# Optimization experiments

Measured on AMD Instinct MI355X. Metric: run time of the kernel, lower is better.

## Reference

```python
import jax, jax.numpy as jnp
import numpy as np

B, T, H, HS, E = 4096, 32, 16, 32, 512  # T == block_size == head_size (required by the module's concat-on-time quirk)


def setup_inputs() -> dict:
    key = jax.random.key(0)
    ks = jax.random.split(key, 6)
    s_e = 1.0 / np.sqrt(E).astype(np.float32)
    s_p = 1.0 / np.sqrt(H * HS).astype(np.float32)
    return {
        "x": jax.random.normal(ks[0], (B, T, E), jnp.float32),
        "Wq": jax.random.normal(ks[1], (H, HS, E), jnp.float32) * s_e,  # per-head Linear(E->HS, no bias)
        "Wk": jax.random.normal(ks[2], (H, HS, E), jnp.float32) * s_e,
        "Wv": jax.random.normal(ks[3], (H, HS, E), jnp.float32) * s_e,
        "Wp": jax.random.normal(ks[4], (E, H * HS), jnp.float32) * s_p,  # proj: Linear(H*HS -> E)
        "bp": jnp.zeros((E,), jnp.float32),
    }


def reference(x, Wq, Wk, Wv, Wp, bp):
    # Per-head projections, batched over heads (original loops in Python).
    q = jnp.einsum('bte,hde->bhtd', x, Wq)  # [B,H,T,HS]
    k = jnp.einsum('bte,hde->bhtd', x, Wk)
    v = jnp.einsum('bte,hde->bhtd', x, Wv)
    wei = jnp.einsum('bhtd,bhsd->bhts', q, k) * (HS ** -0.5)  # [B,H,T,T]
    mask = jnp.tril(jnp.ones((T, T), bool))  # causal (T == block_size)
    wei = jnp.where(mask, wei, -jnp.inf)
    wei = jax.nn.softmax(wei, axis=-1)
    # dropout is identity in eval mode
    out = jnp.einsum('bhts,bhsd->bhtd', wei, v)  # [B,H,T,HS]
    # torch.cat(..., dim=1): stack head outputs along the TIME axis -> [B, H*T, HS]
    out = out.reshape(B, H * T, HS)
    out = jnp.swapaxes(out, 1, 2)  # [B, HS, H*T]; valid only because T == HS -> last dim == H*HS == E
    return out @ Wp.T + bp  # [B, HS, E]
```

## Files before the change

### kernel.cpp

```cpp
#include <hip/hip_runtime.h>
#include <stdint.h>

typedef __attribute__((ext_vector_type(8))) short bf16x8;
typedef __attribute__((ext_vector_type(4))) float f32x4;

#define MFMA16(a, b, c) __builtin_amdgcn_mfma_f32_16x16x32_bf16((a), (b), (c), 0, 0, 0)

__device__ __forceinline__ unsigned short f2bf(float f) {
  unsigned int b = __float_as_uint(f);
  b += 0x7FFFu + ((b >> 16) & 1u);
  return (unsigned short)(b >> 16);
}
__device__ __forceinline__ bf16x8 cvt8(const float4 a, const float4 b) {
  bf16x8 r;
  r[0] = (short)f2bf(a.x); r[1] = (short)f2bf(a.y);
  r[2] = (short)f2bf(a.z); r[3] = (short)f2bf(a.w);
  r[4] = (short)f2bf(b.x); r[5] = (short)f2bf(b.y);
  r[6] = (short)f2bf(b.z); r[7] = (short)f2bf(b.w);
  return r;
}
template <bool BF16W>
__device__ __forceinline__ bf16x8 ldw(const void* p, size_t off) {
  if constexpr (BF16W) {
    return *(const bf16x8*)((const unsigned short*)p + off);
  } else {
    const float* f = (const float*)p + off;
    return cvt8(*(const float4*)f, *(const float4*)(f + 4));
  }
}
__device__ __forceinline__ int sw(int row, int chunk) {
  return row * 512 + ((chunk ^ (row & 7)) << 3);
}

__global__ void cvt_weights_k(const float* __restrict__ wq,
                              const float* __restrict__ wk,
                              const float* __restrict__ wv,
                              const float* __restrict__ wp,
                              unsigned short* __restrict__ dst) {
  const int seg = blockIdx.x >> 7;
  const int blk = blockIdx.x & 127;
  const float* src = (seg == 0) ? wq : (seg == 1) ? wk : (seg == 2) ? wv : wp;
  unsigned short* d = dst + (size_t)seg * 262144;
  const int i = (blk * 256 + threadIdx.x) * 8;
  float4 lo = *(const float4*)&src[i];
  float4 hi = *(const float4*)&src[i + 4];
  *(bf16x8*)&d[i] = cvt8(lo, hi);
}

template <bool BF16W>
__global__ __launch_bounds__(256, 2) void qkv_attn_k(
    const float* __restrict__ x,
    const void* __restrict__ wq,
    const void* __restrict__ wk,
    const void* __restrict__ wv,
    float* __restrict__ y) {
  __shared__ __align__(16) unsigned short Xs[32 * 512];
  __shared__ __align__(16) unsigned short Scr[4][3][32 * 40];
  const int tid  = threadIdx.x;
  const int lane = tid & 63;
  const int wave = tid >> 6;
  const int m    = lane & 15;
  const int quad = lane >> 4;
  const int b    = blockIdx.x;

  {
    const float* xg = x + (size_t)b * (32 * 512);
#pragma unroll
    for (int i = 0; i < 8; i++) {
      int c = tid + 256 * i;
      int row = c >> 6, ch = c & 63;
      float4 lo = *(const float4*)&xg[row * 512 + ch * 8];
      float4 hi = *(const float4*)&xg[row * 512 + ch * 8 + 4];
      *(bf16x8*)&Xs[sw(row, ch)] = cvt8(lo, hi);
    }
  }
  __syncthreads();

  unsigned short* Qs = &Scr[wave][0][0];
  unsigned short* Ks = &Scr[wave][1][0];
  unsigned short* Vt = &Scr[wave][2][0];

  for (int hg = 0; hg < 4; hg++) {
    const int h = hg * 4 + wave;
    f32x4 aq[2][2] = {}; f32x4 ak[2][2] = {}; f32x4 av[2][2] = {};
    const size_t wbase = (size_t)(h * 32 + m) * 512 + quad * 8;
#pragma unroll 4
    for (int kk = 0; kk < 16; kk++) {
      const int k0 = kk * 32;
      bf16x8 a0 = *(const bf16x8*)&Xs[sw(m, kk * 4 + quad)];
      bf16x8 a1 = *(const bf16x8*)&Xs[sw(16 + m, kk * 4 + quad)];
      bf16x8 bq0 = ldw<BF16W>(wq, wbase + k0);
      bf16x8 bq1 = ldw<BF16W>(wq, wbase + 16 * 512 + k0);
      bf16x8 bk0 = ldw<BF16W>(wk, wbase + k0);
      bf16x8 bk1 = ldw<BF16W>(wk, wbase + 16 * 512 + k0);
      bf16x8 bv0 = ldw<BF16W>(wv, wbase + k0);
      bf16x8 bv1 = ldw<BF16W>(wv, wbase + 16 * 512 + k0);
      aq[0][0] = MFMA16(a0, bq0, aq[0][0]);
      aq[1][0] = MFMA16(a1, bq0, aq[1][0]);
      aq[0][1] = MFMA16(a0, bq1, aq[0][1]);
      aq[1][1] = MFMA16(a1, bq1, aq[1][1]);
      ak[0][0] = MFMA16(a0, bk0, ak[0][0]);
      ak[1][0] = MFMA16(a1, bk0, ak[1][0]);
      ak[0][1] = MFMA16(a0, bk1, ak[0][1]);
      ak[1][1] = MFMA16(a1, bk1, ak[1][1]);
      av[0][0] = MFMA16(a0, bv0, av[0][0]);
      av[1][0] = MFMA16(a1, bv0, av[1][0]);
      av[0][1] = MFMA16(a0, bv1, av[0][1]);
      av[1][1] = MFMA16(a1, bv1, av[1][1]);
    }
#pragma unroll
    for (int mi = 0; mi < 2; mi++)
#pragma unroll
      for (int ni = 0; ni < 2; ni++)
#pragma unroll
        for (int r = 0; r < 4; r++) {
          int row = mi * 16 + quad * 4 + r;
          int col = ni * 16 + m;
          Qs[row * 40 + col] = f2bf(aq[mi][ni][r]);
          Ks[row * 40 + col] = f2bf(ak[mi][ni][r]);
          Vt[col * 40 + row] = f2bf(av[mi][ni][r]);
        }
    f32x4 sAcc[2][2];
#pragma unroll
    for (int mi = 0; mi < 2; mi++)
#pragma unroll
      for (int ni = 0; ni < 2; ni++) {
        bf16x8 qa = *(const bf16x8*)&Qs[(mi * 16 + m) * 40 + quad * 8];
        bf16x8 kb = *(const bf16x8*)&Ks[(ni * 16 + m) * 40 + quad * 8];
        f32x4 z = {};
        sAcc[mi][ni] = MFMA16(qa, kb, z);
      }
    float invs[2][4];
#pragma unroll
    for (int mi = 0; mi < 2; mi++)
#pragma unroll
      for (int r = 0; r < 4; r++) {
        int t = mi * 16 + quad * 4 + r;
        float s0 = sAcc[mi][0][r] * 0.17677669529663687f;
        float s1 = sAcc[mi][1][r] * 0.17677669529663687f;
        s0 = (m <= t) ? s0 : -1e30f;
        s1 = (16 + m <= t) ? s1 : -1e30f;
        float mx = fmaxf(s0, s1);
#pragma unroll
        for (int off = 1; off < 16; off <<= 1) mx = fmaxf(mx, __shfl_xor(mx, off));
        float e0 = __expf(s0 - mx);
        float e1 = __expf(s1 - mx);
        float sm = e0 + e1;
#pragma unroll
        for (int off = 1; off < 16; off <<= 1) sm += __shfl_xor(sm, off);
        invs[mi][r] = 1.0f / sm;
        Qs[t * 40 + m] = f2bf(e0);
        Qs[t * 40 + 16 + m] = f2bf(e1);
      }
    f32x4 oAcc[2][2];
#pragma unroll
    for (int mi = 0; mi < 2; mi++)
#pragma unroll
      for (int ni = 0; ni < 2; ni++) {
        bf16x8 pa = *(const bf16x8*)&Qs[(mi * 16 + m) * 40 + quad * 8];
        bf16x8 vb = *(const bf16x8*)&Vt[(ni * 16 + m) * 40 + quad * 8];
        f32x4 z = {};
        oAcc[mi][ni] = MFMA16(pa, vb, z);
      }
#pragma unroll
    for (int mi = 0; mi < 2; mi++)
#pragma unroll
      for (int ni = 0; ni < 2; ni++) {
        float4 o;
        o.x = oAcc[mi][ni][0] * invs[mi][0];
        o.y = oAcc[mi][ni][1] * invs[mi][1];
        o.z = oAcc[mi][ni][2] * invs[mi][2];
        o.w = oAcc[mi][ni][3] * invs[mi][3];
        int d = ni * 16 + m;
        int t0 = mi * 16 + quad * 4;
        *(float4*)&y[(size_t)b * 16384 + (size_t)d * 512 + h * 32 + t0] = o;
      }
  }
}

template <bool BF16W>
__global__ __launch_bounds__(256, 2) void proj_k(
    float* __restrict__ y,
    const void* __restrict__ wp,
    const float* __restrict__ bp) {
  __shared__ __align__(16) unsigned short Ys[64 * 512];
  const int tid  = threadIdx.x;
  const int lane = tid & 63;
  const int wave = tid >> 6;
  const int m    = lane & 15;
  const int quad = lane >> 4;
  const size_t rbase = (size_t)blockIdx.x * 64;

  {
    const float* yg = y + rbase * 512;
#pragma unroll
    for (int i = 0; i < 16; i++) {
      int c = tid + 256 * i;
      int row = c >> 6, ch = c & 63;
      float4 lo = *(const float4*)&yg[row * 512 + ch * 8];
      float4 hi = *(const float4*)&yg[row * 512 + ch * 8 + 4];
      *(bf16x8*)&Ys[sw(row, ch)] = cvt8(lo, hi);
    }
  }
  __syncthreads();

  const int nb = wave * 128;
  f32x4 acc[4][8] = {};
#pragma unroll 2
  for (int kk = 0; kk < 16; kk++) {
    bf16x8 a[4];
#pragma unroll
    for (int mi = 0; mi < 4; mi++)
      a[mi] = *(const bf16x8*)&Ys[sw(mi * 16 + m, kk * 4 + quad)];
    const int k0 = kk * 32 + quad * 8;
#pragma unroll
    for (int ni = 0; ni < 8; ni++) {
      bf16x8 bb = ldw<BF16W>(wp, (size_t)(nb + ni * 16 + m) * 512 + k0);
#pragma unroll
      for (int mi = 0; mi < 4; mi++) acc[mi][ni] = MFMA16(a[mi], bb, acc[mi][ni]);
    }
  }
#pragma unroll
  for (int ni = 0; ni < 8; ni++) {
    const int col = nb + ni * 16 + m;
    const float bias = bp[col];
#pragma unroll
    for (int mi = 0; mi < 4; mi++)
#pragma unroll
      for (int r = 0; r < 4; r++) {
        size_t row = rbase + mi * 16 + quad * 4 + r;
        y[row * 512 + col] = acc[mi][ni][r] + bias;
      }
  }
}

extern "C" void kernel_launch(void* const* d_in, const int* in_sizes, int n_in,
                              void* d_out, int out_size, void* d_ws, size_t ws_size,
                              hipStream_t stream) {
  (void)in_sizes; (void)n_in; (void)out_size;
  const float* x  = (const float*)d_in[0];
  const float* wq = (const float*)d_in[1];
  const float* wk = (const float*)d_in[2];
  const float* wv = (const float*)d_in[3];
  const float* wp = (const float*)d_in[4];
  const float* bp = (const float*)d_in[5];
  float* y = (float*)d_out;

  const size_t WE = 262144;
  if (ws_size >= 4 * WE * sizeof(unsigned short)) {
    unsigned short* wb = (unsigned short*)d_ws;
    cvt_weights_k<<<512, 256, 0, stream>>>(wq, wk, wv, wp, wb);
    qkv_attn_k<true><<<4096, 256, 0, stream>>>(x, wb, wb + WE, wb + 2 * WE, y);
    proj_k<true><<<2048, 256, 0, stream>>>(y, wb + 3 * WE, bp);
  } else {
    qkv_attn_k<false><<<4096, 256, 0, stream>>>(x, wq, wk, wv, y);
    proj_k<false><<<2048, 256, 0, stream>>>(y, wp, bp);
  }
}
```

Baseline: 1.284 ms.

## Double-buffer GEMM operand loads and stagger K/head order across blocks

Both the QKV-attention kernel and the projection kernel now software-pipeline their K loops with two register buffers, loading the next K-slice of LDS activations and global weights while MFMAs run on the current one. In addition, each block starts its K loop (and the head-group loop in the attention kernel) at an offset derived from the block index. The offset spreads concurrent blocks across different weight addresses to reduce cache or channel hot-spotting. The cost is higher register pressure, especially in the projection kernel, which now holds two sets of 4+8 operand vectors next to a 128-float accumulator and may spill or lose occupancy.

```diff
diff --git a/kernel.cpp b/kernel.cpp
--- a/kernel.cpp
+++ b/kernel.cpp
@@ -62,6 +62,8 @@
   const int m    = lane & 15;
   const int quad = lane >> 4;
   const int b    = blockIdx.x;
+  const int koff = (blockIdx.x >> 3) & 15;
+  const int hgo  = (blockIdx.x >> 7) & 3;
 
   {
     const float* xg = x + (size_t)b * (32 * 512);
@@ -81,33 +83,52 @@
   unsigned short* Vt = &Scr[wave][2][0];
 
   for (int hg = 0; hg < 4; hg++) {
-    const int h = hg * 4 + wave;
+    const int h = ((hg + hgo) & 3) * 4 + wave;
     f32x4 aq[2][2] = {}; f32x4 ak[2][2] = {}; f32x4 av[2][2] = {};
     const size_t wbase = (size_t)(h * 32 + m) * 512 + quad * 8;
-#pragma unroll 4
-    for (int kk = 0; kk < 16; kk++) {
-      const int k0 = kk * 32;
-      bf16x8 a0 = *(const bf16x8*)&Xs[sw(m, kk * 4 + quad)];
-      bf16x8 a1 = *(const bf16x8*)&Xs[sw(16 + m, kk * 4 + quad)];
-      bf16x8 bq0 = ldw<BF16W>(wq, wbase + k0);
-      bf16x8 bq1 = ldw<BF16W>(wq, wbase + 16 * 512 + k0);
-      bf16x8 bk0 = ldw<BF16W>(wk, wbase + k0);
-      bf16x8 bk1 = ldw<BF16W>(wk, wbase + 16 * 512 + k0);
-      bf16x8 bv0 = ldw<BF16W>(wv, wbase + k0);
-      bf16x8 bv1 = ldw<BF16W>(wv, wbase + 16 * 512 + k0);
-      aq[0][0] = MFMA16(a0, bq0, aq[0][0]);
-      aq[1][0] = MFMA16(a1, bq0, aq[1][0]);
-      aq[0][1] = MFMA16(a0, bq1, aq[0][1]);
-      aq[1][1] = MFMA16(a1, bq1, aq[1][1]);
-      ak[0][0] = MFMA16(a0, bk0, ak[0][0]);
-      ak[1][0] = MFMA16(a1, bk0, ak[1][0]);
-      ak[0][1] = MFMA16(a0, bk1, ak[0][1]);
-      ak[1][1] = MFMA16(a1, bk1, ak[1][1]);
-      av[0][0] = MFMA16(a0, bv0, av[0][0]);
-      av[1][0] = MFMA16(a1, bv0, av[1][0]);
-      av[0][1] = MFMA16(a0, bv1, av[0][1]);
-      av[1][1] = MFMA16(a1, bv1, av[1][1]);
+
+    bf16x8 a0A, a1A, bq0A, bq1A, bk0A, bk1A, bv0A, bv1A;
+    bf16x8 a0B, a1B, bq0B, bq1B, bk0B, bk1B, bv0B, bv1B;
+
+#define LDF(S, idx) { \
+    const int kx = ((idx) + koff) & 15; \
+    const int kb = kx * 32; \
+    a0##S  = *(const bf16x8*)&Xs[sw(m, kx * 4 + quad)]; \
+    a1##S  = *(const bf16x8*)&Xs[sw(16 + m, kx * 4 + quad)]; \
+    bq0##S = ldw<BF16W>(wq, wbase + kb); \
+    bq1##S = ldw<BF16W>(wq, wbase + 16 * 512 + kb); \
+    bk0##S = ldw<BF16W>(wk, wbase + kb); \
+    bk1##S = ldw<BF16W>(wk, wbase + 16 * 512 + kb); \
+    bv0##S = ldw<BF16W>(wv, wbase + kb); \
+    bv1##S = ldw<BF16W>(wv, wbase + 16 * 512 + kb); }
+
+#define MMF(S) { \
+    aq[0][0] = MFMA16(a0##S, bq0##S, aq[0][0]); \
+    aq[1][0] = MFMA16(a1##S, bq0##S, aq[1][0]); \
+    aq[0][1] = MFMA16(a0##S, bq1##S, aq[0][1]); \
+    aq[1][1] = MFMA16(a1##S, bq1##S, aq[1][1]); \
+    ak[0][0] = MFMA16(a0##S, bk0##S, ak[0][0]); \
+    ak[1][0] = MFMA16(a1##S, bk0##S, ak[1][0]); \
+    ak[0][1] = MFMA16(a0##S, bk1##S, ak[0][1]); \
+    ak[1][1] = MFMA16(a1##S, bk1##S, ak[1][1]); \
+    av[0][0] = MFMA16(a0##S, bv0##S, av[0][0]); \
+    av[1][0] = MFMA16(a1##S, bv0##S, av[1][0]); \
+    av[0][1] = MFMA16(a0##S, bv1##S, av[0][1]); \
+    av[1][1] = MFMA16(a1##S, bv1##S, av[1][1]); }
+
+    LDF(A, 0)
+    for (int i = 0; i < 14; i += 2) {
+      LDF(B, i + 1)
+      MMF(A)
+      LDF(A, i + 2)
+      MMF(B)
     }
+    LDF(B, 15)
+    MMF(A)
+    MMF(B)
+#undef LDF
+#undef MMF
+
 #pragma unroll
     for (int mi = 0; mi < 2; mi++)
 #pragma unroll
@@ -190,6 +211,7 @@
   const int m    = lane & 15;
   const int quad = lane >> 4;
   const size_t rbase = (size_t)blockIdx.x * 64;
+  const int koff = (blockIdx.x >> 3) & 15;
 
   {
     const float* yg = y + rbase * 512;
@@ -206,20 +228,40 @@
 
   const int nb = wave * 128;
   f32x4 acc[4][8] = {};
-#pragma unroll 2
-  for (int kk = 0; kk < 16; kk++) {
-    bf16x8 a[4];
-#pragma unroll
-    for (int mi = 0; mi < 4; mi++)
-      a[mi] = *(const bf16x8*)&Ys[sw(mi * 16 + m, kk * 4 + quad)];
-    const int k0 = kk * 32 + quad * 8;
-#pragma unroll
-    for (int ni = 0; ni < 8; ni++) {
-      bf16x8 bb = ldw<BF16W>(wp, (size_t)(nb + ni * 16 + m) * 512 + k0);
-#pragma unroll
-      for (int mi = 0; mi < 4; mi++) acc[mi][ni] = MFMA16(a[mi], bb, acc[mi][ni]);
-    }
-  }
+  bf16x8 aA[4], aB[4], wA[8], wB[8];
+
+#define K2A(S, idx) { \
+    const int kx = ((idx) + koff) & 15; \
+    _Pragma("unroll") \
+    for (int mi = 0; mi < 4; mi++) \
+      a##S[mi] = *(const bf16x8*)&Ys[sw(mi * 16 + m, kx * 4 + quad)]; }
+#define K2W(S, idx) { \
+    const int kx = ((idx) + koff) & 15; \
+    const int kb = kx * 32 + quad * 8; \
+    _Pragma("unroll") \
+    for (int ni = 0; ni < 8; ni++) \
+      w##S[ni] = ldw<BF16W>(wp, (size_t)(nb + ni * 16 + m) * 512 + kb); }
+#define K2MM(S) { \
+    _Pragma("unroll") \
+    for (int ni = 0; ni < 8; ni++) \
+      _Pragma("unroll") \
+      for (int mi = 0; mi < 4; mi++) \
+        acc[mi][ni] = MFMA16(a##S[mi], w##S[ni], acc[mi][ni]); }
+
+  K2A(A, 0) K2W(A, 0)
+  for (int i = 0; i < 14; i += 2) {
+    K2A(B, i + 1) K2W(B, i + 1)
+    K2MM(A)
+    K2A(A, i + 2) K2W(A, i + 2)
+    K2MM(B)
+  }
+  K2A(B, 15) K2W(B, 15)
+  K2MM(A)
+  K2MM(B)
+#undef K2A
+#undef K2W
+#undef K2MM
+
 #pragma unroll
   for (int ni = 0; ni < 8; ni++) {
     const int col = nb + ni * 16 + m;
```

New measurement: 1.308 ms. No clear change (+1.9%).
